# Performance work log

Hardware: AMD Instinct MI355X
Metric: run time of the kernel (lower is better)

The kernel has to match this reference:

```python
import jax, jax.numpy as jnp
import numpy as np
import math

B, C, L, E, N = 16, 256, 2048, 512, 64
H = 2 * C  # S4 model dimension


def setup_inputs() -> dict:
    key = jax.random.key(0)
    ks = jax.random.split(key, 12)
    inp = {
        "x": jax.random.normal(ks[0], (B, C, L), dtype=jnp.float32),
        "diffusion_emb": jax.random.normal(ks[1], (B, E), dtype=jnp.float32),
        "dp_W": jax.random.normal(ks[2], (C, E), dtype=jnp.float32) / np.sqrt(E).astype(np.float32),
        "dp_b": jnp.zeros((C,), dtype=jnp.float32),
        "in_W": jax.random.normal(ks[3], (H, C), dtype=jnp.float32) / np.sqrt(C).astype(np.float32),
        "in_b": jnp.zeros((H,), dtype=jnp.float32),
        "out_W": jax.random.normal(ks[4], (2 * C, C), dtype=jnp.float32) / np.sqrt(C).astype(np.float32),
        "out_b": jnp.zeros((2 * C,), dtype=jnp.float32),
        "ln1_g": jnp.ones((H,), dtype=jnp.float32),
        "ln1_b": jnp.zeros((H,), dtype=jnp.float32),
        "ln2_g": jnp.ones((H,), dtype=jnp.float32),
        "ln2_b": jnp.zeros((H,), dtype=jnp.float32),
    }
    for i, pre in enumerate(["s41_", "s42_"]):
        k = jax.random.fold_in(key, 100 + i)
        k1, k2, k3, k4, k5 = jax.random.split(k, 5)
        # dt log-uniform in [1e-3, 1e-1] (standard S4 init)
        inp[pre + "log_dt"] = (jax.random.uniform(k1, (H,)) * (math.log(0.1) - math.log(0.001)) + math.log(0.001)).astype(jnp.float32)
        inp[pre + "A_re"] = (-0.5 * jnp.ones((H, N))).astype(jnp.float32)
        inp[pre + "A_im"] = jnp.tile(math.pi * jnp.arange(N, dtype=jnp.float32), (H, 1))
        inp[pre + "C_re"] = jax.random.normal(k2, (H, N), dtype=jnp.float32) * (0.5 ** 0.5)
        inp[pre + "C_im"] = jax.random.normal(k3, (H, N), dtype=jnp.float32) * (0.5 ** 0.5)
        inp[pre + "D"] = jax.random.normal(k4, (H,), dtype=jnp.float32)
        inp[pre + "oW"] = jax.random.normal(k5, (2 * H, H), dtype=jnp.float32) / np.sqrt(H).astype(np.float32)
        inp[pre + "ob"] = jnp.zeros((2 * H,), dtype=jnp.float32)
    return inp


def _s4(u, log_dt, A_re, A_im, C_re, C_im, D, oW, ob):
    # u: [B, H, L]. Diagonal SSM (S4D, ZOH discretization) -> FFT conv -> D skip -> GELU -> GLU output linear.
    Lq = u.shape[-1]
    dt = jnp.exp(log_dt)                       # [H]
    A = A_re + 1j * A_im                       # [H, N] diagonal state matrix
    Cc = C_re + 1j * C_im                      # [H, N]
    dtA = dt[:, None] * A                      # [H, N]
    Ct = Cc * (jnp.exp(dtA) - 1.0) / A         # ZOH-discretized C*B (B = 1)
    lr = jnp.arange(Lq)
    # Vandermonde kernel: K[h, l] = 2 Re sum_n Ct[h, n] exp(dtA[h, n] * l)
    K = 2.0 * jnp.real(jnp.einsum("hn,hnl->hl", Ct, jnp.exp(dtA[:, :, None] * lr)))  # [H, L]
    nfft = 2 * Lq
    y = jnp.fft.irfft(jnp.fft.rfft(u, n=nfft) * jnp.fft.rfft(K, n=nfft), n=nfft)[..., :Lq]
    y = y + D[None, :, None] * u
    y = jax.nn.gelu(y)
    y = jnp.einsum("oh,bhl->bol", oW, y) + ob[None, :, None]  # [B, 2H, L]
    a, b = jnp.split(y, 2, axis=1)             # GLU over channel dim
    return a * jax.nn.sigmoid(b)               # [B, H, L]


def _ln(y, g, b):
    # LayerNorm over the channel dim (module rearranges b c l -> b l c, LN(C), back)
    mu = jnp.mean(y, axis=1, keepdims=True)
    var = jnp.var(y, axis=1, keepdims=True)
    return (y - mu) * jax.lax.rsqrt(var + 1e-5) * g[None, :, None] + b[None, :, None]


def reference(x, diffusion_emb, dp_W, dp_b, in_W, in_b, out_W, out_b,
              ln1_g, ln1_b, ln2_g, ln2_b,
              s41_log_dt, s41_A_re, s41_A_im, s41_C_re, s41_C_im, s41_D, s41_oW, s41_ob,
              s42_log_dt, s42_A_re, s42_A_im, s42_C_re, s42_C_im, s42_D, s42_oW, s42_ob):
    d = diffusion_emb @ dp_W.T + dp_b          # [B, C] -> broadcast as [B, C, 1]
    y = x + d[:, :, None]
    y = jnp.einsum("oc,bcl->bol", in_W, y) + in_b[None, :, None]   # 1x1 conv: [B, 2C, L]
    y = _s4(y, s41_log_dt, s41_A_re, s41_A_im, s41_C_re, s41_C_im, s41_D, s41_oW, s41_ob)
    y = _ln(y, ln1_g, ln1_b)
    y = _s4(y, s42_log_dt, s42_A_re, s42_A_im, s42_C_re, s42_C_im, s42_D, s42_oW, s42_ob)
    y = _ln(y, ln2_g, ln2_b)
    gate, filt = jnp.split(y, 2, axis=1)
    y = jax.nn.sigmoid(gate) * jnp.tanh(filt)  # [B, C, L]
    y = jnp.einsum("oc,bcl->bol", out_W, y) + out_b[None, :, None]  # [B, 2C, L]
    residual, skip = jnp.split(y, 2, axis=1)
    return ((x + residual) / math.sqrt(2.0), skip)
```

## Files before the change

kernel.cpp:

```cpp
#include <hip/hip_runtime.h>
#include <math.h>

#define Bsz 16
#define Cch 256
#define Lsq 2048
#define Emb 512
#define Nst 64
#define Hch 512
#define KGP 2240

typedef _Float16 f16;
typedef _Float16 f16x8 __attribute__((ext_vector_type(8)));
typedef _Float16 f16x4 __attribute__((ext_vector_type(4)));
typedef float f32x4 __attribute__((ext_vector_type(4)));
typedef uint32_t u32x4 __attribute__((ext_vector_type(4)));

__device__ __forceinline__ float sigmoidf_(float x) { return 1.0f/(1.0f + __expf(-x)); }
__device__ __forceinline__ float gelu_tanh(float y) {
  float z = 0.7978845608028654f*(y + 0.044715f*y*y*y);
  float zc = fminf(fmaxf(z, -12.f), 12.f);
  float e = __expf(2.f*zc);
  return y - y/(e + 1.f);
}

__device__ __forceinline__ void gload_lds16(const f16* g, f16* l) {
  __builtin_amdgcn_global_load_lds(
      (const __attribute__((address_space(1))) void*)g,
      (__attribute__((address_space(3))) void*)l, 16, 0, 0);
}


__global__ void k_emb(const float* __restrict__ emb, const float* __restrict__ dpW,
                      const float* __restrict__ dpb, float* __restrict__ d) {
  int b = blockIdx.x, c = threadIdx.x;
  const float* e = emb + b*Emb;
  const float* w = dpW + c*Emb;
  float s = dpb[c];
  for (int k = 0; k < Emb; ++k) s += e[k]*w[k];
  d[b*Cch + c] = s;
}

__global__ void k_f2h(const float* __restrict__ src, f16* __restrict__ dst, int n) {
  int i = blockIdx.x*256 + threadIdx.x;
  if (i < n) dst[i] = (f16)src[i];
}

__global__ void k_addemb(const float* __restrict__ x, const float* __restrict__ d,
                         f16* __restrict__ xd) {
  int i = blockIdx.x*256 + threadIdx.x;
  const float4* x4 = (const float4*)x;
  float4 v = x4[i];
  int bc = (i*4)/Lsq;
  float dd = d[bc];
  f16x4 o;
  o[0] = (f16)(v.x+dd); o[1] = (f16)(v.y+dd); o[2] = (f16)(v.z+dd); o[3] = (f16)(v.w+dd);
  ((f16x4*)xd)[i] = o;
}

__global__ void k_s4prep(const float* __restrict__ log_dt,
                         const float* __restrict__ A_re, const float* __restrict__ A_im,
                         const float* __restrict__ C_re, const float* __restrict__ C_im,
                         float* __restrict__ w_re, float* __restrict__ w_im,
                         float* __restrict__ ccr, float* __restrict__ cci) {
  int i = blockIdx.x*256 + threadIdx.x;
  if (i >= Hch*Nst) return;
  int h = i >> 6;
  float dt = expf(log_dt[h]);
  float Ar = A_re[i], Ai = A_im[i];
  float er = expf(dt*Ar);
  float wr = er*cosf(dt*Ai), wi = er*sinf(dt*Ai);
  float mag = Ar*Ar + Ai*Ai;
  float nr = wr - 1.0f, ni = wi;
  float qr = (nr*Ar + ni*Ai)/mag, qi = (ni*Ar - nr*Ai)/mag;
  float cr = C_re[i], ci = C_im[i];
  float tr = cr*qr - ci*qi, ti = cr*qi + ci*qr;
  w_re[i] = wr; w_im[i] = wi; ccr[i] = 2.0f*tr; cci[i] = -2.0f*ti;
}

__global__ __launch_bounds__(256) void k_kgen(
    const float* __restrict__ w_re, const float* __restrict__ w_im,
    const float* __restrict__ ccr, const float* __restrict__ cci,
    const float* __restrict__ Dvec,
    f16* __restrict__ Ke, f16* __restrict__ Ko) {
  __shared__ float2 wbt[64][65];
  __shared__ float2 wat[32][66];
  __shared__ float2 ccs[64];
  __shared__ float Kf[2048];
  int h = blockIdx.x, tid = threadIdx.x;
  if (tid < 64) {
    int n = tid;
    double wr = (double)w_re[h*64+n], wi = (double)w_im[h*64+n];
    double br = 1.0, bi = 0.0;
    for (int j = 0; j < 64; ++j) {
      wbt[n][j] = make_float2((float)br, (float)bi);
      double t = br*wr - bi*wi; bi = br*wi + bi*wr; br = t;
    }
    double ar = 1.0, ai = 0.0;
    for (int a = 0; a < 32; ++a) {
      wat[a][n] = make_float2((float)ar, (float)ai);
      double t = ar*br - ai*bi; ai = ar*bi + ai*br; ar = t;
    }
    ccs[n] = make_float2(ccr[h*64+n], cci[h*64+n]);
  }
  __syncthreads();
  int lane = tid & 63, wv = tid >> 6;
  float acc[8] = {0.f,0.f,0.f,0.f,0.f,0.f,0.f,0.f};
  for (int n = 0; n < 64; ++n) {
    float2 wb = wbt[n][lane];
    float2 cc = ccs[n];
    float tr = fmaf(cc.y, wb.y,  cc.x*wb.x);
    float ti = fmaf(cc.y, wb.x, -cc.x*wb.y);
    #pragma unroll
    for (int li = 0; li < 8; ++li) {
      float2 wa = wat[wv + 4*li][n];
      acc[li] = fmaf(wa.x, tr, acc[li]);
      acc[li] = fmaf(wa.y, ti, acc[li]);
    }
  }
  #pragma unroll
  for (int li = 0; li < 8; ++li)
    Kf[(wv + 4*li)*64 + lane] = acc[li];
  __syncthreads();
  if (tid == 0) Kf[0] += Dvec[h];
  __syncthreads();
  f16* keh = Ke + (size_t)h*KGP;
  f16* koh = Ko + (size_t)h*KGP;
  for (int q = tid; q < KGP; q += 256) {
    float e = (q < 2048) ? Kf[2047 - q] : 0.f;
    float o = (q < 2047) ? Kf[2046 - q] : 0.f;
    keh[q] = (f16)e; koh[q] = (f16)o;
  }
}

__device__ __forceinline__ f16x8 ld4u32(const uint32_t* __restrict__ p) {
  union { uint32_t u[4]; f16x8 v; } r;
  r.u[0] = p[0]; r.u[1] = p[1]; r.u[2] = p[2]; r.u[3] = p[3];
  return r.v;
}

__global__ __launch_bounds__(512) void k_conv(
    const f16* __restrict__ u, const f16* __restrict__ Ke, const f16* __restrict__ Ko,
    f16* __restrict__ g) {
  __shared__ __align__(16) f16 Ul[16*2048];
  int h = blockIdx.x, tid = threadIdx.x;
  {
    int b = tid >> 5, pr = tid & 31;
    const f16* src = u + ((size_t)b*Hch + h)*Lsq;
    f16* dst = &Ul[b*2048];
    #pragma unroll
    for (int c = 0; c < 8; ++c) {
      int gs = c*32 + pr;
      *(f16x8*)&dst[(gs ^ b)*8] = *(const f16x8*)(src + gs*8);
    }
  }
  __syncthreads();
  int wv = tid >> 6, lane = tid & 63;
  int m = lane & 15, qd = lane >> 4;
  const f16* keh = Ke + (size_t)h*KGP;
  const f16* koh = Ko + (size_t)h*KGP;
  const uint32_t* kb = (m & 1) ? (const uint32_t*)keh : (const uint32_t*)koh;
  f16* gb = g + ((size_t)m*Hch + h)*Lsq;
  const f16* ulb = &Ul[m*2048];
  for (int pi = 0; pi < 2; ++pi) {
    int P = pi ? (15 - wv) : wv;
    int i0 = P*128;
    int qb0 = 2047 - i0 - m + qd*8;
    int ib = qb0 >> 1;
    f32x4 acc[8];
    #pragma unroll
    for (int t = 0; t < 8; ++t) acc[t] = (f32x4){0.f,0.f,0.f,0.f};
    f16x8 W[8];
    #pragma unroll
    for (int t = 0; t < 8; ++t) W[t] = ld4u32(kb + ib - 8*t);
    int steps = 4*(P+1);
    for (int s4i = 0; s4i < steps; s4i += 4) {
      const uint32_t* pw = kb + ib + 16*(s4i + 1);
      #pragma unroll
      for (int ph = 0; ph < 4; ++ph) {
        int s = s4i + ph;
        f16x8 bf = *(const f16x8*)&ulb[((4*s + qd) ^ m)*8];
        f16x8 nf0 = ld4u32(pw + 16*ph);
        f16x8 nf1 = ld4u32(pw + 16*ph - 8);
        __builtin_amdgcn_s_setprio(1);
        #pragma unroll
        for (int t = 0; t < 8; ++t)
          acc[t] = __builtin_amdgcn_mfma_f32_16x16x32_f16(W[(t - 2*ph) & 7], bf, acc[t], 0, 0, 0);
        __builtin_amdgcn_s_setprio(0);
        W[(6 - 2*ph) & 7] = nf0;
        W[(7 - 2*ph) & 7] = nf1;
      }
    }
    #pragma unroll
    for (int t = 0; t < 8; ++t) {
      f16x4 o;
      #pragma unroll
      for (int r = 0; r < 4; ++r) o[r] = (f16)gelu_tanh(acc[t][r]);
      *(f16x4*)&gb[i0 + 16*t + qd*4] = o;
    }
  }
}

template<int KD, int MODE>
__global__ __launch_bounds__(512) void k_gemm(
    const f16* __restrict__ W, const f16* __restrict__ Bact,
    const float* __restrict__ bias, const float* __restrict__ xres,
    float* __restrict__ outF, f16* __restrict__ outH) {
  constexpr int TOFF = (MODE == 1) ? 512 : 256;
  constexpr int NK = KD/32;
  constexpr int MT = (MODE == 1) ? 4 : 2;
  __shared__ __align__(16) f16 As[2][128*8*8];
  __shared__ __align__(16) uint32_t Bs[2][16*260];
  int tid = threadIdx.x;
  int wv = tid >> 6, lane = tid & 63;

  int nwg = 128*MT;
  int bid = blockIdx.x;
  int lin = (bid & 7)*(nwg >> 3) + (bid >> 3);
  int mt = lin % MT;
  int nt = lin / MT;
  int bb = nt >> 3;
  int l0 = (nt & 7)*256;
  int m0 = mt*128;
  int wm = (wv & 1)*64, wn = (wv >> 1)*64;
  int qd = lane >> 4, ln16 = lane & 15;

  f32x4 acc[2][4][4];
  #pragma unroll
  for (int t = 0; t < 2; ++t)
    for (int i = 0; i < 4; ++i)
      for (int j = 0; j < 4; ++j)
        acc[t][i][j] = (f32x4){0.f,0.f,0.f,0.f};

  const f16* Bbase = Bact + (size_t)bb*KD*Lsq + l0;
  int q16 = tid >> 5, nch = tid & 31;

  auto stageA = [&](int buf, int kk) {
    #pragma unroll
    for (int i = 0; i < 2; ++i) {
      int gbase = (wv*2 + i)*64;
      int G = gbase + lane;
      int row = G >> 3;
      int gsw = (G & 7) ^ (row & 7);
      int t = gsw >> 2;
      const f16* src = W + (size_t)(m0 + row + t*TOFF)*KD + kk + (gsw & 3)*8;
      gload_lds16(src, &As[buf][gbase*8]);
    }
  };
  f16x8 rb0, rb1;
  auto loadB = [&](int kk) {
    const f16* b0 = Bbase + (size_t)(kk + 2*q16)*Lsq + nch*8;
    rb0 = *(const f16x8*)b0;
    rb1 = *(const f16x8*)(b0 + Lsq);
  };
  auto packB = [&](int buf) {
    union { uint32_t w[8]; u32x4 v[2]; } pk;
    #pragma unroll
    for (int e = 0; e < 8; ++e) {
      union { f16 h2[2]; uint32_t u; } t2;
      t2.h2[0] = rb0[e]; t2.h2[1] = rb1[e];
      pk.w[e] = t2.u;
    }
    *(u32x4*)&Bs[buf][q16*260 + nch*8]     = pk.v[0];
    *(u32x4*)&Bs[buf][q16*260 + nch*8 + 4] = pk.v[1];
  };
  auto compute = [&](int buf) {
    f16x8 afr[2][4];
    #pragma unroll
    for (int i = 0; i < 4; ++i)
      for (int t = 0; t < 2; ++t) {
        int row = wm + i*16 + ln16;
        int g = (t*4 + qd) ^ (row & 7);
        afr[t][i] = *(const f16x8*)&As[buf][(row*8 + g)*8];
      }
    f16x8 bfr[4];
    #pragma unroll
    for (int j = 0; j < 4; ++j) {
      union { uint32_t w2[4]; f16x8 v; } bu;
      #pragma unroll
      for (int r2 = 0; r2 < 4; ++r2) bu.w2[r2] = Bs[buf][(qd*4 + r2)*260 + wn + j*16 + ln16];
      bfr[j] = bu.v;
    }
    __builtin_amdgcn_s_setprio(1);
    #pragma unroll
    for (int j = 0; j < 4; ++j)
      for (int i = 0; i < 4; ++i)
        for (int t = 0; t < 2; ++t)
          acc[t][i][j] = __builtin_amdgcn_mfma_f32_16x16x32_f16(afr[t][i], bfr[j], acc[t][i][j], 0, 0, 0);
    __builtin_amdgcn_s_setprio(0);
  };

  stageA(0, 0);
  loadB(0);
  packB(0);
  __syncthreads();

  int cur = 0;
  for (int t = 0; t < NK; ++t) {
    if (t + 1 < NK) {
      stageA(cur ^ 1, (t + 1)*32);
      loadB((t + 1)*32);
    }
    compute(cur);
    if (t + 1 < NK) packB(cur ^ 1);
    __syncthreads();
    cur ^= 1;
  }

  #pragma unroll
  for (int i = 0; i < 4; ++i)
    for (int j = 0; j < 4; ++j)
      for (int r = 0; r < 4; ++r) {
        int ml = wm + i*16 + qd*4 + r;
        int nl = wn + j*16 + ln16;
        int mg = m0 + ml;
        int l  = l0 + nl;
        if (MODE == 0) {
          outH[((size_t)bb*Hch + mg)*Lsq + l]       = (f16)(acc[0][i][j][r] + bias[mg]);
          outH[((size_t)bb*Hch + mg + 256)*Lsq + l] = (f16)(acc[1][i][j][r] + bias[mg + 256]);
        } else if (MODE == 1) {
          float va = acc[0][i][j][r] + bias[mg];
          float vb = acc[1][i][j][r] + bias[512 + mg];
          outH[((size_t)bb*Hch + mg)*Lsq + l] = (f16)(va * sigmoidf_(vb));
        } else {
          size_t idx = ((size_t)bb*Cch + mg)*Lsq + l;
          float v0 = acc[0][i][j][r] + bias[mg];
          outF[idx] = (v0 + xres[idx]) * 0.7071067811865476f;
          float v1 = acc[1][i][j][r] + bias[mg + 256];
          outF[(size_t)Bsz*Cch*Lsq + idx] = v1;
        }
      }
}

template<int MODE>
__global__ __launch_bounds__(256) void k_ln(const f16* __restrict__ v,
                                            const float* __restrict__ gam, const float* __restrict__ bet,
                                            float* __restrict__ outF, f16* __restrict__ outH) {
  __shared__ float red[2][4][64];
  int b = blockIdx.x >> 5;
  int l = (blockIdx.x & 31)*64 + (threadIdx.x & 63);
  int wv = threadIdx.x >> 6, lane = threadIdx.x & 63;
  const f16* base = v + (size_t)b*Hch*Lsq + l;
  float s = 0.f, s2 = 0.f;
  for (int h = wv*128; h < wv*128 + 128; ++h) {
    float xv = (float)base[(size_t)h*Lsq];
    s += xv; s2 += xv*xv;
  }
  red[0][wv][lane] = s; red[1][wv][lane] = s2;
  __syncthreads();
  s  = red[0][0][lane] + red[0][1][lane] + red[0][2][lane] + red[0][3][lane];
  s2 = red[1][0][lane] + red[1][1][lane] + red[1][2][lane] + red[1][3][lane];
  float mu = s*(1.0f/Hch);
  float var = s2*(1.0f/Hch) - mu*mu;
  float rs = rsqrtf(var + 1e-5f);
  if (MODE == 0) {
    f16* ob = outH + (size_t)b*Hch*Lsq + l;
    for (int h = wv*128; h < wv*128 + 128; ++h)
      ob[(size_t)h*Lsq] = (f16)(((float)base[(size_t)h*Lsq] - mu)*rs*gam[h] + bet[h]);
  } else {
    f16* ob = outH + (size_t)b*Cch*Lsq + l;
    for (int c = wv*64; c < wv*64 + 64; ++c) {
      float xg = ((float)base[(size_t)c*Lsq] - mu)*rs*gam[c] + bet[c];
      float xf = ((float)base[(size_t)(c+Cch)*Lsq] - mu)*rs*gam[c+Cch] + bet[c+Cch];
      float xfc = fminf(fmaxf(xf, -15.f), 15.f);
      float e = __expf(2.f*xfc);
      ob[(size_t)c*Lsq] = (f16)(sigmoidf_(xg) * ((e-1.f)/(e+1.f)));
    }
  }
}

extern "C" void kernel_launch(void* const* d_in, const int* in_sizes, int n_in,
                              void* d_out, int out_size, void* d_ws, size_t ws_size,
                              hipStream_t stream) {
  const float* x    = (const float*)d_in[0];
  const float* emb  = (const float*)d_in[1];
  const float* dpW  = (const float*)d_in[2];
  const float* dpb  = (const float*)d_in[3];
  const float* inW  = (const float*)d_in[4];
  const float* inb  = (const float*)d_in[5];
  const float* outW = (const float*)d_in[6];
  const float* outb = (const float*)d_in[7];
  const float* ln1g = (const float*)d_in[8];
  const float* ln1b = (const float*)d_in[9];
  const float* ln2g = (const float*)d_in[10];
  const float* ln2b = (const float*)d_in[11];
  const float* s4[2][8];
  for (int ly = 0; ly < 2; ++ly)
    for (int k = 0; k < 8; ++k) s4[ly][k] = (const float*)d_in[12 + ly*8 + k];

  char* p = (char*)d_ws;
  auto alloc = [&](size_t bytes) { char* r = p; p += (bytes + 255) & ~(size_t)255; return r; };
  f16* inW16  = (f16*)alloc((size_t)Hch*Cch*2);
  f16* oW16_0 = (f16*)alloc((size_t)2*Hch*Hch*2);
  f16* oW16_1 = (f16*)alloc((size_t)2*Hch*Hch*2);
  f16* outW16 = (f16*)alloc((size_t)2*Cch*Cch*2);
  float* dbuf = (float*)alloc((size_t)Bsz*Cch*4);
  float* prm[2][4];
  for (int ly = 0; ly < 2; ++ly)
    for (int k = 0; k < 4; ++k) prm[ly][k] = (float*)alloc((size_t)Hch*Nst*4);
  f16* kge[2], *kgo[2];
  for (int ly = 0; ly < 2; ++ly) {
    kge[ly] = (f16*)alloc((size_t)Hch*KGP*2);
    kgo[ly] = (f16*)alloc((size_t)Hch*KGP*2);
  }
  f16*  xd   = (f16*)alloc((size_t)Bsz*Cch*Lsq*2);
  f16*  u16g = (f16*)alloc((size_t)Bsz*Hch*Lsq*2);
  f16*  gbuf = (f16*)alloc((size_t)Bsz*Hch*Lsq*2);
  f16*  glu  = (f16*)alloc((size_t)Bsz*Hch*Lsq*2);
  f16*  oW16[2] = {oW16_0, oW16_1};

  k_emb<<<Bsz, Cch, 0, stream>>>(emb, dpW, dpb, dbuf);
  k_f2h<<<(Hch*Cch+255)/256, 256, 0, stream>>>(inW, inW16, Hch*Cch);
  k_f2h<<<(2*Hch*Hch+255)/256, 256, 0, stream>>>(s4[0][6], oW16_0, 2*Hch*Hch);
  k_f2h<<<(2*Hch*Hch+255)/256, 256, 0, stream>>>(s4[1][6], oW16_1, 2*Hch*Hch);
  k_f2h<<<(2*Cch*Cch+255)/256, 256, 0, stream>>>(outW, outW16, 2*Cch*Cch);
  for (int ly = 0; ly < 2; ++ly) {
    k_s4prep<<<(Hch*Nst+255)/256, 256, 0, stream>>>(s4[ly][0], s4[ly][1], s4[ly][2],
        s4[ly][3], s4[ly][4], prm[ly][0], prm[ly][1], prm[ly][2], prm[ly][3]);
    k_kgen<<<Hch, 256, 0, stream>>>(prm[ly][0], prm[ly][1], prm[ly][2], prm[ly][3],
        s4[ly][5], kge[ly], kgo[ly]);
  }
  k_addemb<<<(Bsz*Cch*Lsq/4)/256, 256, 0, stream>>>(x, dbuf, xd);

  dim3 bl(512);
  k_gemm<Cch, 0><<<256, bl, 0, stream>>>(inW16, xd, inb, nullptr, nullptr, u16g);
  k_conv<<<Hch, 512, 0, stream>>>(u16g, kge[0], kgo[0], gbuf);
  k_gemm<Hch, 1><<<512, bl, 0, stream>>>(oW16[0], gbuf, s4[0][7], nullptr, nullptr, glu);
  k_ln<0><<<Bsz*32, 256, 0, stream>>>(glu, ln1g, ln1b, nullptr, u16g);
  k_conv<<<Hch, 512, 0, stream>>>(u16g, kge[1], kgo[1], gbuf);
  k_gemm<Hch, 1><<<512, bl, 0, stream>>>(oW16[1], gbuf, s4[1][7], nullptr, nullptr, glu);
  k_ln<1><<<Bsz*32, 256, 0, stream>>>(glu, ln2g, ln2b, nullptr, xd);
  k_gemm<Cch, 2><<<256, bl, 0, stream>>>(outW16, xd, outb, x, (float*)d_out, nullptr);
}
```

Before: 503.2 us.

## Retile GEMM to 256x128 tiles and move GLU gating into LayerNorm kernel

The GEMM switches from a 128-row tile that paired two weight halves (for GLU) to a single 256x128 tile with a swizzled B layout in LDS and an occupancy hint in launch_bounds. Grid size doubles and accumulator registers halve. The GLU sigmoid gating moves from the GEMM epilogue into the LayerNorm kernel, which now reads both halves from a doubled intermediate buffer using vectorized f16x4 loads. The intent is to lower register pressure and LDS padding and to vectorize LN memory access, at the cost of writing and then reading twice as much intermediate data.

```diff
diff --git a/kernel.cpp b/kernel.cpp
--- a/kernel.cpp
+++ b/kernel.cpp
@@ -21,6 +21,11 @@
   float zc = fminf(fmaxf(z, -12.f), 12.f);
   float e = __expf(2.f*zc);
   return y - y/(e + 1.f);
+}
+__device__ __forceinline__ float tanhf_(float x) {
+  float xc = fminf(fmaxf(x, -15.f), 15.f);
+  float e = __expf(2.f*xc);
+  return (e - 1.f)/(e + 1.f);
 }
 
 __device__ __forceinline__ void gload_lds16(const f16* g, f16* l) {
@@ -201,91 +206,91 @@
 }
 
 template<int KD, int MODE>
-__global__ __launch_bounds__(512) void k_gemm(
+__global__ __launch_bounds__(512, 4) void k_gemm(
     const f16* __restrict__ W, const f16* __restrict__ Bact,
     const float* __restrict__ bias, const float* __restrict__ xres,
     float* __restrict__ outF, f16* __restrict__ outH) {
-  constexpr int TOFF = (MODE == 1) ? 512 : 256;
   constexpr int NK = KD/32;
   constexpr int MT = (MODE == 1) ? 4 : 2;
   __shared__ __align__(16) f16 As[2][128*8*8];
-  __shared__ __align__(16) uint32_t Bs[2][16*260];
+  __shared__ __align__(16) uint32_t Bs[2][16*128];
   int tid = threadIdx.x;
   int wv = tid >> 6, lane = tid & 63;
 
-  int nwg = 128*MT;
+  int nwg = 256*MT;
   int bid = blockIdx.x;
   int lin = (bid & 7)*(nwg >> 3) + (bid >> 3);
   int mt = lin % MT;
   int nt = lin / MT;
-  int bb = nt >> 3;
-  int l0 = (nt & 7)*256;
-  int m0 = mt*128;
-  int wm = (wv & 1)*64, wn = (wv >> 1)*64;
+  int bb = nt >> 4;
+  int l0 = (nt & 15)*128;
+  int m0 = mt*256;
+  int wm = (wv & 3)*64, wn = (wv >> 2)*64;
   int qd = lane >> 4, ln16 = lane & 15;
 
-  f32x4 acc[2][4][4];
+  f32x4 acc[4][4];
   #pragma unroll
-  for (int t = 0; t < 2; ++t)
-    for (int i = 0; i < 4; ++i)
-      for (int j = 0; j < 4; ++j)
-        acc[t][i][j] = (f32x4){0.f,0.f,0.f,0.f};
+  for (int i = 0; i < 4; ++i)
+    for (int j = 0; j < 4; ++j)
+      acc[i][j] = (f32x4){0.f,0.f,0.f,0.f};
 
   const f16* Bbase = Bact + (size_t)bb*KD*Lsq + l0;
   int q16 = tid >> 5, nch = tid & 31;
+  int bswz = (q16 & 7)*4;
 
   auto stageA = [&](int buf, int kk) {
     #pragma unroll
     for (int i = 0; i < 2; ++i) {
       int gbase = (wv*2 + i)*64;
       int G = gbase + lane;
-      int row = G >> 3;
-      int gsw = (G & 7) ^ (row & 7);
-      int t = gsw >> 2;
-      const f16* src = W + (size_t)(m0 + row + t*TOFF)*KD + kk + (gsw & 3)*8;
+      int rp = G >> 3, slot = G & 7;
+      int g = slot ^ (rp & 7);
+      int row = rp*2 + (g >> 2), kg = g & 3;
+      const f16* src = W + (size_t)(m0 + row)*KD + kk + kg*8;
       gload_lds16(src, &As[buf][gbase*8]);
     }
   };
-  f16x8 rb0, rb1;
+  f16x4 rb0, rb1;
   auto loadB = [&](int kk) {
-    const f16* b0 = Bbase + (size_t)(kk + 2*q16)*Lsq + nch*8;
-    rb0 = *(const f16x8*)b0;
-    rb1 = *(const f16x8*)(b0 + Lsq);
+    const f16* b0 = Bbase + (size_t)(kk + 2*q16)*Lsq + nch*4;
+    rb0 = *(const f16x4*)b0;
+    rb1 = *(const f16x4*)(b0 + Lsq);
   };
   auto packB = [&](int buf) {
-    union { uint32_t w[8]; u32x4 v[2]; } pk;
-    #pragma unroll
-    for (int e = 0; e < 8; ++e) {
+    union { uint32_t w[4]; u32x4 v; } pk;
+    #pragma unroll
+    for (int e = 0; e < 4; ++e) {
       union { f16 h2[2]; uint32_t u; } t2;
       t2.h2[0] = rb0[e]; t2.h2[1] = rb1[e];
       pk.w[e] = t2.u;
     }
-    *(u32x4*)&Bs[buf][q16*260 + nch*8]     = pk.v[0];
-    *(u32x4*)&Bs[buf][q16*260 + nch*8 + 4] = pk.v[1];
+    *(u32x4*)&Bs[buf][q16*128 + ((nch*4) ^ bswz)] = pk.v;
   };
   auto compute = [&](int buf) {
-    f16x8 afr[2][4];
-    #pragma unroll
-    for (int i = 0; i < 4; ++i)
-      for (int t = 0; t < 2; ++t) {
-        int row = wm + i*16 + ln16;
-        int g = (t*4 + qd) ^ (row & 7);
-        afr[t][i] = *(const f16x8*)&As[buf][(row*8 + g)*8];
-      }
+    f16x8 afr[4];
+    #pragma unroll
+    for (int i = 0; i < 4; ++i) {
+      int row = wm + i*16 + ln16;
+      int rp = row >> 1;
+      int slot = (((row & 1)*4 + qd)) ^ (rp & 7);
+      afr[i] = *(const f16x8*)&As[buf][(rp*8 + slot)*8];
+    }
     f16x8 bfr[4];
     #pragma unroll
     for (int j = 0; j < 4; ++j) {
       union { uint32_t w2[4]; f16x8 v; } bu;
       #pragma unroll
-      for (int r2 = 0; r2 < 4; ++r2) bu.w2[r2] = Bs[buf][(qd*4 + r2)*260 + wn + j*16 + ln16];
+      for (int r2 = 0; r2 < 4; ++r2) {
+        int kp = qd*4 + r2;
+        bu.w2[r2] = Bs[buf][kp*128 + ((wn + j*16 + ln16) ^ ((kp & 7)*4))];
+      }
       bfr[j] = bu.v;
     }
     __builtin_amdgcn_s_setprio(1);
     #pragma unroll
     for (int j = 0; j < 4; ++j)
       for (int i = 0; i < 4; ++i)
-        for (int t = 0; t < 2; ++t)
-          acc[t][i][j] = __builtin_amdgcn_mfma_f32_16x16x32_f16(afr[t][i], bfr[j], acc[t][i][j], 0, 0, 0);
+        acc[i][j] = __builtin_amdgcn_mfma_f32_16x16x32_f16(afr[i], bfr[j], acc[i][j], 0, 0, 0);
     __builtin_amdgcn_s_setprio(0);
   };
 
@@ -315,55 +320,95 @@
         int mg = m0 + ml;
         int l  = l0 + nl;
         if (MODE == 0) {
-          outH[((size_t)bb*Hch + mg)*Lsq + l]       = (f16)(acc[0][i][j][r] + bias[mg]);
-          outH[((size_t)bb*Hch + mg + 256)*Lsq + l] = (f16)(acc[1][i][j][r] + bias[mg + 256]);
+          outH[((size_t)bb*Hch + mg)*Lsq + l] = (f16)(acc[i][j][r] + bias[mg]);
         } else if (MODE == 1) {
-          float va = acc[0][i][j][r] + bias[mg];
-          float vb = acc[1][i][j][r] + bias[512 + mg];
-          outH[((size_t)bb*Hch + mg)*Lsq + l] = (f16)(va * sigmoidf_(vb));
+          outH[((size_t)bb*1024 + mg)*Lsq + l] = (f16)(acc[i][j][r] + bias[mg]);
         } else {
-          size_t idx = ((size_t)bb*Cch + mg)*Lsq + l;
-          float v0 = acc[0][i][j][r] + bias[mg];
-          outF[idx] = (v0 + xres[idx]) * 0.7071067811865476f;
-          float v1 = acc[1][i][j][r] + bias[mg + 256];
-          outF[(size_t)Bsz*Cch*Lsq + idx] = v1;
+          float v = acc[i][j][r] + bias[mg];
+          if (mg < Cch) {
+            size_t idx = ((size_t)bb*Cch + mg)*Lsq + l;
+            outF[idx] = (v + xres[idx]) * 0.7071067811865476f;
+          } else {
+            size_t idx = ((size_t)bb*Cch + (mg - Cch))*Lsq + l;
+            outF[(size_t)Bsz*Cch*Lsq + idx] = v;
+          }
         }
       }
 }
 
 template<int MODE>
-__global__ __launch_bounds__(256) void k_ln(const f16* __restrict__ v,
+__global__ __launch_bounds__(256) void k_ln(const f16* __restrict__ y,
                                             const float* __restrict__ gam, const float* __restrict__ bet,
                                             float* __restrict__ outF, f16* __restrict__ outH) {
-  __shared__ float red[2][4][64];
+  __shared__ float ps[16][64], ps2[16][64];
+  __shared__ float muL[64], rsL[64];
+  int tid = threadIdx.x;
   int b = blockIdx.x >> 5;
-  int l = (blockIdx.x & 31)*64 + (threadIdx.x & 63);
-  int wv = threadIdx.x >> 6, lane = threadIdx.x & 63;
-  const f16* base = v + (size_t)b*Hch*Lsq + l;
-  float s = 0.f, s2 = 0.f;
-  for (int h = wv*128; h < wv*128 + 128; ++h) {
-    float xv = (float)base[(size_t)h*Lsq];
-    s += xv; s2 += xv*xv;
-  }
-  red[0][wv][lane] = s; red[1][wv][lane] = s2;
-  __syncthreads();
-  s  = red[0][0][lane] + red[0][1][lane] + red[0][2][lane] + red[0][3][lane];
-  s2 = red[1][0][lane] + red[1][1][lane] + red[1][2][lane] + red[1][3][lane];
-  float mu = s*(1.0f/Hch);
-  float var = s2*(1.0f/Hch) - mu*mu;
-  float rs = rsqrtf(var + 1e-5f);
+  int l0 = (blockIdx.x & 31)*64;
+  int wv = tid >> 6, lane = tid & 63;
+  int hh = lane >> 4;
+  int lq = (lane & 15)*4;
+  const f16* yb = y + (size_t)b*1024*Lsq + l0 + lq;
+  float s[4] = {0.f,0.f,0.f,0.f}, t2[4] = {0.f,0.f,0.f,0.f};
+  for (int it = 0; it < 32; ++it) {
+    int c = wv*128 + it*4 + hh;
+    f16x4 a = *(const f16x4*)(yb + (size_t)c*Lsq);
+    f16x4 f = *(const f16x4*)(yb + (size_t)(c + 512)*Lsq);
+    #pragma unroll
+    for (int j = 0; j < 4; ++j) {
+      float gv = (float)a[j] * sigmoidf_((float)f[j]);
+      s[j] += gv; t2[j] += gv*gv;
+    }
+  }
+  #pragma unroll
+  for (int j = 0; j < 4; ++j) { ps[wv*4 + hh][lq + j] = s[j]; ps2[wv*4 + hh][lq + j] = t2[j]; }
+  __syncthreads();
+  if (tid < 64) {
+    float ss = 0.f, s2 = 0.f;
+    #pragma unroll
+    for (int p = 0; p < 16; ++p) { ss += ps[p][tid]; s2 += ps2[p][tid]; }
+    float mu = ss*(1.0f/Hch);
+    float var = s2*(1.0f/Hch) - mu*mu;
+    muL[tid] = mu; rsL[tid] = rsqrtf(var + 1e-5f);
+  }
+  __syncthreads();
+  float mu4[4], rs4[4];
+  #pragma unroll
+  for (int j = 0; j < 4; ++j) { mu4[j] = muL[lq + j]; rs4[j] = rsL[lq + j]; }
   if (MODE == 0) {
-    f16* ob = outH + (size_t)b*Hch*Lsq + l;
-    for (int h = wv*128; h < wv*128 + 128; ++h)
-      ob[(size_t)h*Lsq] = (f16)(((float)base[(size_t)h*Lsq] - mu)*rs*gam[h] + bet[h]);
+    f16* ob = outH + (size_t)b*Hch*Lsq + l0 + lq;
+    for (int it = 0; it < 32; ++it) {
+      int c = wv*128 + it*4 + hh;
+      f16x4 a = *(const f16x4*)(yb + (size_t)c*Lsq);
+      f16x4 f = *(const f16x4*)(yb + (size_t)(c + 512)*Lsq);
+      float gc = gam[c], bc = bet[c];
+      f16x4 o;
+      #pragma unroll
+      for (int j = 0; j < 4; ++j) {
+        float gv = (float)a[j] * sigmoidf_((float)f[j]);
+        o[j] = (f16)((gv - mu4[j])*rs4[j]*gc + bc);
+      }
+      *(f16x4*)(ob + (size_t)c*Lsq) = o;
+    }
   } else {
-    f16* ob = outH + (size_t)b*Cch*Lsq + l;
-    for (int c = wv*64; c < wv*64 + 64; ++c) {
-      float xg = ((float)base[(size_t)c*Lsq] - mu)*rs*gam[c] + bet[c];
-      float xf = ((float)base[(size_t)(c+Cch)*Lsq] - mu)*rs*gam[c+Cch] + bet[c+Cch];
-      float xfc = fminf(fmaxf(xf, -15.f), 15.f);
-      float e = __expf(2.f*xfc);
-      ob[(size_t)c*Lsq] = (f16)(sigmoidf_(xg) * ((e-1.f)/(e+1.f)));
+    f16* ob = outH + (size_t)b*Cch*Lsq + l0 + lq;
+    for (int it = 0; it < 16; ++it) {
+      int c = wv*64 + it*4 + hh;
+      f16x4 a1 = *(const f16x4*)(yb + (size_t)c*Lsq);
+      f16x4 f1 = *(const f16x4*)(yb + (size_t)(c + 512)*Lsq);
+      f16x4 a2 = *(const f16x4*)(yb + (size_t)(c + 256)*Lsq);
+      f16x4 f2 = *(const f16x4*)(yb + (size_t)(c + 768)*Lsq);
+      float g1 = gam[c], b1 = bet[c], g2 = gam[c + 256], b2 = bet[c + 256];
+      f16x4 o;
+      #pragma unroll
+      for (int j = 0; j < 4; ++j) {
+        float gv1 = (float)a1[j] * sigmoidf_((float)f1[j]);
+        float gv2 = (float)a2[j] * sigmoidf_((float)f2[j]);
+        float n1 = (gv1 - mu4[j])*rs4[j]*g1 + b1;
+        float n2 = (gv2 - mu4[j])*rs4[j]*g2 + b2;
+        o[j] = (f16)(sigmoidf_(n1) * tanhf_(n2));
+      }
+      *(f16x4*)(ob + (size_t)c*Lsq) = o;
     }
   }
 }
@@ -405,7 +450,7 @@
   f16*  xd   = (f16*)alloc((size_t)Bsz*Cch*Lsq*2);
   f16*  u16g = (f16*)alloc((size_t)Bsz*Hch*Lsq*2);
   f16*  gbuf = (f16*)alloc((size_t)Bsz*Hch*Lsq*2);
-  f16*  glu  = (f16*)alloc((size_t)Bsz*Hch*Lsq*2);
+  f16*  ybuf = (f16*)alloc((size_t)Bsz*2*Hch*Lsq*2);
   f16*  oW16[2] = {oW16_0, oW16_1};
 
   k_emb<<<Bsz, Cch, 0, stream>>>(emb, dpW, dpb, dbuf);
@@ -422,12 +467,12 @@
   k_addemb<<<(Bsz*Cch*Lsq/4)/256, 256, 0, stream>>>(x, dbuf, xd);
 
   dim3 bl(512);
-  k_gemm<Cch, 0><<<256, bl, 0, stream>>>(inW16, xd, inb, nullptr, nullptr, u16g);
+  k_gemm<Cch, 0><<<512, bl, 0, stream>>>(inW16, xd, inb, nullptr, nullptr, u16g);
   k_conv<<<Hch, 512, 0, stream>>>(u16g, kge[0], kgo[0], gbuf);
-  k_gemm<Hch, 1><<<512, bl, 0, stream>>>(oW16[0], gbuf, s4[0][7], nullptr, nullptr, glu);
-  k_ln<0><<<Bsz*32, 256, 0, stream>>>(glu, ln1g, ln1b, nullptr, u16g);
+  k_gemm<Hch, 1><<<1024, bl, 0, stream>>>(oW16[0], gbuf, s4[0][7], nullptr, nullptr, ybuf);
+  k_ln<0><<<Bsz*32, 256, 0, stream>>>(ybuf, ln1g, ln1b, nullptr, u16g);
   k_conv<<<Hch, 512, 0, stream>>>(u16g, kge[1], kgo[1], gbuf);
-  k_gemm<Hch, 1><<<512, bl, 0, stream>>>(oW16[1], gbuf, s4[1][7], nullptr, nullptr, glu);
-  k_ln<1><<<Bsz*32, 256, 0, stream>>>(glu, ln2g, ln2b, nullptr, xd);
-  k_gemm<Cch, 2><<<256, bl, 0, stream>>>(outW16, xd, outb, x, (float*)d_out, nullptr);
-}
+  k_gemm<Hch, 1><<<1024, bl, 0, stream>>>(oW16[1], gbuf, s4[1][7], nullptr, nullptr, ybuf);
+  k_ln<1><<<Bsz*32, 256, 0, stream>>>(ybuf, ln2g, ln2b, nullptr, xd);
+  k_gemm<Cch, 2><<<512, bl, 0, stream>>>(outW16, xd, outb, x, (float*)d_out, nullptr);
+}
```

Result: slower. 561.1 us (+11.5%).
